# Performance work log

Hardware: AMD Instinct MI355X
Metric: run time of the kernel (lower is better)

The kernel has to match this reference:

```python
import jax, jax.numpy as jnp
import numpy as np

N, E, C, NB = 10000, 160000, 32, 8  # atoms, edges, channels, radial basis


def _W(k, shp):
    return jax.random.normal(k, shp, jnp.float32) / np.float32(np.sqrt(shp[0]))


def setup_inputs():
    ks = jax.random.split(jax.random.key(0), 16)
    return {
        "p1": jax.random.normal(ks[0], (N, C), jnp.float32),
        "p3": jax.random.normal(ks[1], (N, 3, C), jnp.float32),
        "r3": jax.random.normal(ks[2], (E, 3), jnp.float32),
        "basis": jax.random.normal(ks[3], (E, NB), jnp.float32),
        "idx_i": jax.random.randint(ks[4], (E,), 0, N, jnp.int32),
        "idx_j": jax.random.randint(ks[5], (E,), 0, N, jnp.int32),
        "pp1_W": _W(ks[6], (C, C)), "pp1_b": jnp.zeros((C,), jnp.float32),
        "pi1_W1": _W(ks[7], (2 * C, C)), "pi1_b1": jnp.zeros((C,), jnp.float32),
        "pi1_W2": _W(ks[8], (C, 3 * C)), "pi1_b2": jnp.zeros((3 * C,), jnp.float32),
        "pi1_W3": _W(ks[9], (3 * C, 3 * C * NB)),
        "ii1_W": _W(ks[10], (C, C)), "ii1_b": jnp.zeros((C,), jnp.float32),
        "pp3_W": _W(ks[11], (C, C)), "pp3_b": jnp.zeros((C,), jnp.float32),
        "pi3_W1": _W(ks[12], (2 * C, C)), "pi3_b1": jnp.zeros((C,), jnp.float32),
        "pi3_W2": _W(ks[13], (C, C)), "pi3_b2": jnp.zeros((C,), jnp.float32),
        "pi3_W3": _W(ks[14], (C, C * NB)),
        "ii3_W": _W(ks[15], (C, C)), "ii3_b": jnp.zeros((C,), jnp.float32),
    }


def _pi_layer(prop, idx_i, idx_j, basis, W1, b1, W2, b2, W3, out_c):
    # gather both endpoints, concat, linear MLP (no activation, no last bias),
    # contract trailing basis axis with per-edge basis functions
    inter = jnp.concatenate([prop[idx_i], prop[idx_j]], axis=-1)  # [E, ..., 2C]
    h = inter @ W1 + b1
    h = h @ W2 + b2
    h = h @ W3                                   # [E, ..., out_c*NB]
    h = h.reshape(h.shape[:-1] + (out_c, NB))
    return jnp.einsum('e...cb,eb->e...c', h, basis)


def _forward(p1, p3, r3, basis, idx_i, idx_j,
             pp1_W, pp1_b, pi1_W1, pi1_b1, pi1_W2, pi1_b2, pi1_W3, ii1_W, ii1_b,
             pp3_W, pp3_b, pi3_W1, pi3_b1, pi3_W2, pi3_b2, pi3_W3, ii3_W, ii3_b):
    act = jnp.tanh
    # rank-1 branch
    p1h = act(p1 @ pp1_W + pp1_b)                                   # [N, C]
    i1 = _pi_layer(p1h, idx_i, idx_j, basis,
                   pi1_W1, pi1_b1, pi1_W2, pi1_b2, pi1_W3, 3 * C)   # [E, 3C]
    i1_1, i1_2, i1_3 = jnp.split(i1, 3, axis=-1)
    i1a = act(i1_1 @ ii1_W + ii1_b)                                  # [E, C]
    p1n = jax.ops.segment_sum(i1a, idx_j, num_segments=N)            # [N, C]
    # rank-3 (vector) branch
    p3h = act(p3 @ pp3_W + pp3_b)                                    # [N, 3, C]
    i3 = _pi_layer(p3h, idx_i, idx_j, basis,
                   pi3_W1, pi3_b1, pi3_W2, pi3_b2, pi3_W3, C)        # [E, 3, C]
    i3 = act(i3 @ ii3_W + ii3_b)
    # equivariant scale/add: i3*i1_2 + r3*i1_3 (broadcast over Cartesian axis)
    i3 = i3 * i1_2[:, None, :] + r3[:, :, None] * i1_3[:, None, :]   # [E, 3, C]
    p3n = jax.ops.segment_sum(i3, idx_j, num_segments=N)             # [N, 3, C]
    # dot layer + residual into p1, then rescale p3 by p1
    p1o = jnp.sum(p3n * p3n, axis=1) + p1n                           # [N, C]
    p3o = p3n * p1o[:, None, :]                                      # [N, 3, C]
    return p1o, p3o


def reference(p1, p3, r3, basis, idx_i, idx_j,
              pp1_W, pp1_b, pi1_W1, pi1_b1, pi1_W2, pi1_b2, pi1_W3, ii1_W, ii1_b,
              pp3_W, pp3_b, pi3_W1, pi3_b1, pi3_W2, pi3_b2, pi3_W3, ii3_W, ii3_b):
    return _forward(p1, p3, r3, basis, idx_i, idx_j,
                    pp1_W, pp1_b, pi1_W1, pi1_b1, pi1_W2, pi1_b2, pi1_W3, ii1_W, ii1_b,
                    pp3_W, pp3_b, pi3_W1, pi3_b1, pi3_W2, pi3_b2, pi3_W3, ii3_W, ii3_b)
```

## Files before the change

### kernel.cpp

```cpp
#include <hip/hip_runtime.h>
#include <math.h>

#define NN 10000
#define NE 160000

typedef __attribute__((ext_vector_type(8))) short s8v;
typedef __attribute__((ext_vector_type(4))) float f4v;
typedef unsigned short u16;

#define OFF_P1HB 0u
#define OFF_P3HB 640000u
#define OFF_WB   2560000u
#define OFF_SCR  2703360u
#define OFF_P1N  2736640u
#define OFF_P3N  4016640u

#define OWF1  0
#define OBB1  49152
#define OII1T 52224
#define OWF3  53248
#define OBB3  69632
#define OII3T 70656
#define NWB   71680

__device__ __forceinline__ short f2b(float f) {
    unsigned u = __float_as_uint(f);
    u += 0x7fffu + ((u >> 16) & 1u);
    return (short)(u >> 16);
}
__device__ __forceinline__ float tanhf_fast(float x) {
    float xc = fminf(9.f, fmaxf(-9.f, x));
    float e = __expf(2.f * xc);
    return (e - 1.f) * __builtin_amdgcn_rcpf(e + 1.f);
}

__global__ __launch_bounds__(256) void node_prep(
    const float* __restrict__ p1, const float* __restrict__ p3,
    const float* __restrict__ pp1_W, const float* __restrict__ pp1_b,
    const float* __restrict__ pp3_W, const float* __restrict__ pp3_b,
    u16* __restrict__ p1hb, u16* __restrict__ p3hb)
{
    __shared__ float Ws[2][32 * 32];
    __shared__ float bsm[2][32];
    int tid = threadIdx.x;
    for (int i = tid; i < 32 * 32; i += 256) { Ws[0][i] = pp1_W[i]; Ws[1][i] = pp3_W[i]; }
    if (tid < 32) { bsm[0][tid] = pp1_b[tid]; bsm[1][tid] = pp3_b[tid]; }
    __syncthreads();
    int idx = blockIdx.x * 256 + tid;
    int n = idx >> 7;
    int r = (idx >> 5) & 3;
    int c = idx & 31;
    int sel = (r == 0) ? 0 : 1;
    const float* in = (r == 0) ? (p1 + n * 32) : (p3 + (n * 3 + (r - 1)) * 32);
    float acc = bsm[sel][c];
    #pragma unroll
    for (int k = 0; k < 32; ++k) acc += in[k] * Ws[sel][k * 32 + c];
    short v = f2b(tanhf(acc));
    if (r == 0) p1hb[n * 32 + c] = (u16)v;
    else        p3hb[(n * 3 + (r - 1)) * 32 + c] = (u16)v;
}

__global__ __launch_bounds__(256) void wprep1(
    const float* __restrict__ W1, const float* __restrict__ W2,
    const float* __restrict__ b1, const float* __restrict__ b2,
    const float* __restrict__ W13, const float* __restrict__ W23,
    const float* __restrict__ b13, const float* __restrict__ b23,
    float* __restrict__ scr)
{
    float* T1  = scr;
    float* T3  = scr + 6144;
    float* bt1 = scr + 8192;
    float* bt3 = scr + 8288;
    int i = blockIdx.x * 256 + threadIdx.x;
    if (i < 6144) {
        int r = i / 96, c = i % 96;
        float a = 0.f;
        #pragma unroll 8
        for (int k = 0; k < 32; ++k) a += W1[r * 32 + k] * W2[k * 96 + c];
        T1[i] = a;
    } else if ((i -= 6144) < 2048) {
        int r = i / 32, c = i % 32;
        float a = 0.f;
        #pragma unroll 8
        for (int k = 0; k < 32; ++k) a += W13[r * 32 + k] * W23[k * 32 + c];
        T3[i] = a;
    } else if ((i -= 2048) < 96) {
        float a = b2[i];
        #pragma unroll 8
        for (int k = 0; k < 32; ++k) a += b1[k] * W2[k * 96 + i];
        bt1[i] = a;
    } else if ((i -= 96) < 32) {
        float a = b23[i];
        #pragma unroll 8
        for (int k = 0; k < 32; ++k) a += b13[k] * W23[k * 32 + i];
        bt3[i] = a;
    }
}

__global__ __launch_bounds__(256) void wprep2(
    const float* __restrict__ W3, const float* __restrict__ W33,
    const float* __restrict__ ii1, const float* __restrict__ ii3,
    const float* __restrict__ scr, u16* __restrict__ wb)
{
    const float* T1  = scr;
    const float* T3  = scr + 6144;
    const float* bt1 = scr + 8192;
    const float* bt3 = scr + 8288;
    int i0 = blockIdx.x * 256 + threadIdx.x;
    if (i0 >= NWB) return;
    int i = i0;
    float v = 0.f;
    if (i < 49152) {
        int b = i / 6144, r = i % 6144;
        int nt = r / 1024, r2 = r % 1024;
        int ks = r2 / 512, r3 = r2 & 511;
        int L = r3 >> 3, j = r3 & 7;
        int k = ks * 32 + (L >> 4) * 8 + j;
        int c = 16 * nt + (L & 15);
        float a = 0.f;
        #pragma unroll 8
        for (int q = 0; q < 96; ++q) a += T1[k * 96 + q] * W3[q * 768 + c * 8 + b];
        v = a;
    } else if ((i -= 49152) < 3072) {
        int nt = i / 512, r3 = i & 511;
        int L = r3 >> 3, j = r3 & 7;
        if ((L >> 4) == 0) {
            int x = (16 * nt + (L & 15)) * 8 + j;
            float a = 0.f;
            #pragma unroll 8
            for (int q = 0; q < 96; ++q) a += bt1[q] * W3[q * 768 + x];
            v = a;
        }
    } else if ((i -= 3072) < 1024) {
        int nt = i / 512, r3 = i & 511;
        int L = r3 >> 3, j = r3 & 7;
        v = ii1[((L >> 4) * 8 + j) * 32 + 16 * nt + (L & 15)];
    } else if ((i -= 1024) < 16384) {
        int b = i / 2048, r = i % 2048;
        int nt = r / 1024, r2 = r % 1024;
        int ks = r2 / 512, r3 = r2 & 511;
        int L = r3 >> 3, j = r3 & 7;
        int k = ks * 32 + (L >> 4) * 8 + j;
        int c = 16 * nt + (L & 15);
        float a = 0.f;
        #pragma unroll 8
        for (int q = 0; q < 32; ++q) a += T3[k * 32 + q] * W33[q * 256 + c * 8 + b];
        v = a;
    } else if ((i -= 16384) < 1024) {
        int nt = i / 512, r3 = i & 511;
        int L = r3 >> 3, j = r3 & 7;
        if ((L >> 4) == 0) {
            int x = (16 * nt + (L & 15)) * 8 + j;
            float a = 0.f;
            #pragma unroll 8
            for (int q = 0; q < 32; ++q) a += bt3[q] * W33[q * 256 + x];
            v = a;
        }
    } else {
        i -= 1024;
        int nt = i / 512, r3 = i & 511;
        int L = r3 >> 3, j = r3 & 7;
        v = ii3[((L >> 4) * 8 + j) * 32 + 16 * nt + (L & 15)];
    }
    wb[i0] = (u16)f2b(v);
}

__global__ __launch_bounds__(64, 3) void edge_kernel(
    const u16* __restrict__ p1hb, const u16* __restrict__ p3hb,
    const float* __restrict__ r3, const float* __restrict__ basis,
    const int* __restrict__ idx_i, const int* __restrict__ idx_j,
    const u16* __restrict__ wb,
    const float* __restrict__ ii1b, const float* __restrict__ ii3b,
    float* __restrict__ p1n, float* __restrict__ p3n)
{
    __shared__ int4 smem4[192];
    char* sw = (char*)smem4;
    int*   sIdxI = (int*)(sw + 0);
    int*   sIdxJ = (int*)(sw + 128);
    float* sBasT = (float*)(sw + 256);
    float* sR3   = (float*)(sw + 1280);
    u16*   sT2   = (u16*)(sw + 1664);

    const int l   = threadIdx.x & 63;
    const int r16 = l & 15;
    const int kg  = l >> 4;
    const int ebase = blockIdx.x * 32;

    if (l < 32) sIdxI[l] = idx_i[ebase + l];
    else        sIdxJ[l - 32] = idx_j[ebase + l - 32];
    {
        int e = l & 31, hf = l >> 5;
        const float4* bp = (const float4*)(basis + (size_t)(ebase + e) * 8);
        float4 q = bp[hf];
        sBasT[(4 * hf + 0) * 32 + e] = q.x;
        sBasT[(4 * hf + 1) * 32 + e] = q.y;
        sBasT[(4 * hf + 2) * 32 + e] = q.z;
        sBasT[(4 * hf + 3) * 32 + e] = q.w;
        if (hf == 0) {
            sR3[e]      = r3[(size_t)(ebase + e) * 3 + 0];
            sR3[32 + e] = r3[(size_t)(ebase + e) * 3 + 1];
            sR3[64 + e] = r3[(size_t)(ebase + e) * 3 + 2];
        }
    }

    const float vii1[2] = { ii1b[r16], ii1b[16 + r16] };
    const float vii3[2] = { ii3b[r16], ii3b[16 + r16] };

    const f4v zf = {0.f, 0.f, 0.f, 0.f};

    s8v bA[2];
    #pragma unroll
    for (int m = 0; m < 2; ++m) {
        s8v t;
        #pragma unroll
        for (int j = 0; j < 8; ++j)
            t[j] = (kg == 0) ? f2b(sBasT[j * 32 + m * 16 + r16]) : (short)0;
        bA[m] = t;
    }

    s8v avI[2], avJ[2];
    #pragma unroll
    for (int m = 0; m < 2; ++m) {
        int rowA = m * 16 + r16;
        avI[m] = *(const s8v*)(p1hb + (size_t)sIdxI[rowA] * 32 + kg * 8);
        avJ[m] = *(const s8v*)(p1hb + (size_t)sIdxJ[rowA] * 32 + kg * 8);
    }

    f4v accT[2][6];
    {
        const u16* gBB = wb + OBB1;
        #pragma unroll
        for (int nt = 0; nt < 6; ++nt) {
            s8v bbv = *(const s8v*)(gBB + (nt * 64 + l) * 8);
            #pragma unroll
            for (int m = 0; m < 2; ++m)
                accT[m][nt] = __builtin_amdgcn_mfma_f32_16x16x32_bf16(bA[m], bbv, zf, 0, 0, 0);
        }
    }

    {
        const u16* gW = wb + OWF1;
        #pragma unroll 2
        for (int b = 0; b < 8; ++b) {
            float tb[2][4];
            #pragma unroll
            for (int m = 0; m < 2; ++m)
                #pragma unroll
                for (int rr = 0; rr < 4; ++rr)
                    tb[m][rr] = sBasT[b * 32 + m * 16 + 4 * kg + rr];
            #pragma unroll
            for (int nt = 0; nt < 6; ++nt) {
                const u16* bp = gW + ((size_t)(b * 6 + nt) * 2) * 512 + l * 8;
                s8v bv0 = *(const s8v*)(bp);
                s8v bv1 = *(const s8v*)(bp + 512);
                #pragma unroll
                for (int m = 0; m < 2; ++m) {
                    f4v D = __builtin_amdgcn_mfma_f32_16x16x32_bf16(avI[m], bv0, zf, 0, 0, 0);
                    D = __builtin_amdgcn_mfma_f32_16x16x32_bf16(avJ[m], bv1, D, 0, 0, 0);
                    #pragma unroll
                    for (int rr = 0; rr < 4; ++rr)
                        accT[m][nt][rr] += tb[m][rr] * D[rr];
                }
            }
        }
    }

    {
        const u16* gII = wb + OII1T;
        #pragma unroll
        for (int m = 0; m < 2; ++m) {
            #pragma unroll
            for (int nt = 0; nt < 2; ++nt)
                #pragma unroll
                for (int rr = 0; rr < 4; ++rr)
                    sT2[(4 * kg + rr) * 40 + 16 * nt + r16] = (u16)f2b(accT[m][nt][rr]);
            s8v av = *(const s8v*)(sT2 + r16 * 40 + 8 * kg);
            #pragma unroll
            for (int nt = 0; nt < 2; ++nt) {
                s8v bv = *(const s8v*)(gII + (nt * 64 + l) * 8);
                f4v ia = __builtin_amdgcn_mfma_f32_16x16x32_bf16(av, bv, zf, 0, 0, 0);
                #pragma unroll
                for (int rr = 0; rr < 4; ++rr) {
                    int rowD = m * 16 + 4 * kg + rr;
                    atomicAdd(&p1n[(size_t)sIdxJ[rowD] * 32 + 16 * nt + r16],
                              tanhf_fast(ia[rr] + vii1[nt]));
                }
            }
        }
    }

    const u16* gW3  = wb + OWF3;
    const u16* gBB3 = wb + OBB3;
    const u16* gII3 = wb + OII3T;
    for (int d = 0; d < 3; ++d) {
        s8v avI3[2], avJ3[2];
        #pragma unroll
        for (int m = 0; m < 2; ++m) {
            int rowA = m * 16 + r16;
            avI3[m] = *(const s8v*)(p3hb + ((size_t)sIdxI[rowA] * 3 + d) * 32 + kg * 8);
            avJ3[m] = *(const s8v*)(p3hb + ((size_t)sIdxJ[rowA] * 3 + d) * 32 + kg * 8);
        }
        f4v accP[2][2];
        #pragma unroll
        for (int nt = 0; nt < 2; ++nt) {
            s8v bbv = *(const s8v*)(gBB3 + (nt * 64 + l) * 8);
            #pragma unroll
            for (int m = 0; m < 2; ++m)
                accP[m][nt] = __builtin_amdgcn_mfma_f32_16x16x32_bf16(bA[m], bbv, zf, 0, 0, 0);
        }
        #pragma unroll 2
        for (int b = 0; b < 8; ++b) {
            float tb[2][4];
            #pragma unroll
            for (int m = 0; m < 2; ++m)
                #pragma unroll
                for (int rr = 0; rr < 4; ++rr)
                    tb[m][rr] = sBasT[b * 32 + m * 16 + 4 * kg + rr];
            #pragma unroll
            for (int nt = 0; nt < 2; ++nt) {
                const u16* bp = gW3 + ((size_t)(b * 2 + nt) * 2) * 512 + l * 8;
                s8v bv0 = *(const s8v*)(bp);
                s8v bv1 = *(const s8v*)(bp + 512);
                #pragma unroll
                for (int m = 0; m < 2; ++m) {
                    f4v D = __builtin_amdgcn_mfma_f32_16x16x32_bf16(avI3[m], bv0, zf, 0, 0, 0);
                    D = __builtin_amdgcn_mfma_f32_16x16x32_bf16(avJ3[m], bv1, D, 0, 0, 0);
                    #pragma unroll
                    for (int rr = 0; rr < 4; ++rr)
                        accP[m][nt][rr] += tb[m][rr] * D[rr];
                }
            }
        }
        #pragma unroll
        for (int m = 0; m < 2; ++m) {
            #pragma unroll
            for (int nt = 0; nt < 2; ++nt)
                #pragma unroll
                for (int rr = 0; rr < 4; ++rr)
                    sT2[(4 * kg + rr) * 40 + 16 * nt + r16] = (u16)f2b(accP[m][nt][rr]);
            s8v av = *(const s8v*)(sT2 + r16 * 40 + 8 * kg);
            #pragma unroll
            for (int nt = 0; nt < 2; ++nt) {
                s8v bv = *(const s8v*)(gII3 + (nt * 64 + l) * 8);
                f4v ja = __builtin_amdgcn_mfma_f32_16x16x32_bf16(av, bv, zf, 0, 0, 0);
                #pragma unroll
                for (int rr = 0; rr < 4; ++rr) {
                    int rowD = m * 16 + 4 * kg + rr;
                    float i3a = tanhf_fast(ja[rr] + vii3[nt]);
                    float val = i3a * accT[m][2 + nt][rr] + sR3[d * 32 + rowD] * accT[m][4 + nt][rr];
                    atomicAdd(&p3n[((size_t)sIdxJ[rowD] * 3 + d) * 32 + 16 * nt + r16], val);
                }
            }
        }
    }
}

__global__ __launch_bounds__(256) void finalize_kernel(
    const float* __restrict__ p1n, const float* __restrict__ p3n,
    float* __restrict__ out)
{
    int t = blockIdx.x * 256 + threadIdx.x;
    int n = t >> 5, c = t & 31;
    float a0 = p3n[(n * 3 + 0) * 32 + c];
    float a1 = p3n[(n * 3 + 1) * 32 + c];
    float a2 = p3n[(n * 3 + 2) * 32 + c];
    float p1o = p1n[t] + a0 * a0 + a1 * a1 + a2 * a2;
    out[t] = p1o;
    float* o3 = out + NN * 32;
    o3[(n * 3 + 0) * 32 + c] = a0 * p1o;
    o3[(n * 3 + 1) * 32 + c] = a1 * p1o;
    o3[(n * 3 + 2) * 32 + c] = a2 * p1o;
}

extern "C" void kernel_launch(void* const* d_in, const int* in_sizes, int n_in,
                              void* d_out, int out_size, void* d_ws, size_t ws_size,
                              hipStream_t stream) {
    const float* p1     = (const float*)d_in[0];
    const float* p3     = (const float*)d_in[1];
    const float* r3     = (const float*)d_in[2];
    const float* basis  = (const float*)d_in[3];
    const int*   idx_i  = (const int*)d_in[4];
    const int*   idx_j  = (const int*)d_in[5];
    const float* pp1_W  = (const float*)d_in[6];
    const float* pp1_b  = (const float*)d_in[7];
    const float* pi1_W1 = (const float*)d_in[8];
    const float* pi1_b1 = (const float*)d_in[9];
    const float* pi1_W2 = (const float*)d_in[10];
    const float* pi1_b2 = (const float*)d_in[11];
    const float* pi1_W3 = (const float*)d_in[12];
    const float* ii1_W  = (const float*)d_in[13];
    const float* ii1_b  = (const float*)d_in[14];
    const float* pp3_W  = (const float*)d_in[15];
    const float* pp3_b  = (const float*)d_in[16];
    const float* pi3_W1 = (const float*)d_in[17];
    const float* pi3_b1 = (const float*)d_in[18];
    const float* pi3_W2 = (const float*)d_in[19];
    const float* pi3_b2 = (const float*)d_in[20];
    const float* pi3_W3 = (const float*)d_in[21];
    const float* ii3_W  = (const float*)d_in[22];
    const float* ii3_b  = (const float*)d_in[23];

    char* ws = (char*)d_ws;
    u16*   p1hb = (u16*)(ws + OFF_P1HB);
    u16*   p3hb = (u16*)(ws + OFF_P3HB);
    u16*   wb   = (u16*)(ws + OFF_WB);
    float* scr  = (float*)(ws + OFF_SCR);
    float* p1n  = (float*)(ws + OFF_P1N);
    float* p3n  = (float*)(ws + OFF_P3N);

    hipMemsetAsync(p1n, 0, 5120000, stream);

    node_prep<<<dim3(5000), dim3(256), 0, stream>>>(p1, p3, pp1_W, pp1_b, pp3_W, pp3_b, p1hb, p3hb);
    wprep1<<<dim3(33), dim3(256), 0, stream>>>(
        pi1_W1, pi1_W2, pi1_b1, pi1_b2, pi3_W1, pi3_W2, pi3_b1, pi3_b2, scr);
    wprep2<<<dim3(NWB / 256), dim3(256), 0, stream>>>(
        pi1_W3, pi3_W3, ii1_W, ii3_W, scr, wb);

    edge_kernel<<<dim3(NE / 32), dim3(64), 0, stream>>>(
        p1hb, p3hb, r3, basis, idx_i, idx_j, wb,
        ii1_b, ii3_b, p1n, p3n);

    finalize_kernel<<<dim3(1250), dim3(256), 0, stream>>>(p1n, p3n, (float*)d_out);
}
```

Before: 136.9 us.

## Fuse node prep, weight folding and accumulator zeroing into one prep kernel

Merges the node projection kernel, the two weight-folding kernels and the memset into a single launch, with block ranges handling each job. The weight folding is reassociated as W1·(W2·W3 column slice) per block using shared memory, which removes the scratch round-trip and the dependency between wprep1 and wprep2. The aim is to cut launch and serialization overhead ahead of the edge kernel. The cost is a larger shared allocation per block, which can lower occupancy for the node-prep blocks, and more complex indexing.

Measured after the change: 133.1 us. 2.8% less time.

```diff
diff --git a/kernel.cpp b/kernel.cpp
--- a/kernel.cpp
+++ b/kernel.cpp
@@ -11,7 +11,6 @@
 #define OFF_P1HB 0u
 #define OFF_P3HB 640000u
 #define OFF_WB   2560000u
-#define OFF_SCR  2703360u
 #define OFF_P1N  2736640u
 #define OFF_P3N  4016640u
 
@@ -34,135 +33,163 @@
     return (e - 1.f) * __builtin_amdgcn_rcpf(e + 1.f);
 }
 
-__global__ __launch_bounds__(256) void node_prep(
+__global__ __launch_bounds__(256) void prep_kernel(
     const float* __restrict__ p1, const float* __restrict__ p3,
     const float* __restrict__ pp1_W, const float* __restrict__ pp1_b,
     const float* __restrict__ pp3_W, const float* __restrict__ pp3_b,
-    u16* __restrict__ p1hb, u16* __restrict__ p3hb)
+    const float* __restrict__ W1, const float* __restrict__ W2,
+    const float* __restrict__ W3,
+    const float* __restrict__ b1v, const float* __restrict__ b2v,
+    const float* __restrict__ ii1,
+    const float* __restrict__ W13, const float* __restrict__ W23,
+    const float* __restrict__ W33,
+    const float* __restrict__ b13v, const float* __restrict__ b23v,
+    const float* __restrict__ ii3,
+    u16* __restrict__ p1hb, u16* __restrict__ p3hb,
+    u16* __restrict__ wb, float* __restrict__ p1n)
 {
-    __shared__ float Ws[2][32 * 32];
-    __shared__ float bsm[2][32];
-    int tid = threadIdx.x;
-    for (int i = tid; i < 32 * 32; i += 256) { Ws[0][i] = pp1_W[i]; Ws[1][i] = pp3_W[i]; }
-    if (tid < 32) { bsm[0][tid] = pp1_b[tid]; bsm[1][tid] = pp3_b[tid]; }
-    __syncthreads();
-    int idx = blockIdx.x * 256 + tid;
-    int n = idx >> 7;
-    int r = (idx >> 5) & 3;
-    int c = idx & 31;
-    int sel = (r == 0) ? 0 : 1;
-    const float* in = (r == 0) ? (p1 + n * 32) : (p3 + (n * 3 + (r - 1)) * 32);
-    float acc = bsm[sel][c];
-    #pragma unroll
-    for (int k = 0; k < 32; ++k) acc += in[k] * Ws[sel][k * 32 + c];
-    short v = f2b(tanhf(acc));
-    if (r == 0) p1hb[n * 32 + c] = (u16)v;
-    else        p3hb[(n * 3 + (r - 1)) * 32 + c] = (u16)v;
-}
-
-__global__ __launch_bounds__(256) void wprep1(
-    const float* __restrict__ W1, const float* __restrict__ W2,
-    const float* __restrict__ b1, const float* __restrict__ b2,
-    const float* __restrict__ W13, const float* __restrict__ W23,
-    const float* __restrict__ b13, const float* __restrict__ b23,
-    float* __restrict__ scr)
-{
-    float* T1  = scr;
-    float* T3  = scr + 6144;
-    float* bt1 = scr + 8192;
-    float* bt3 = scr + 8288;
-    int i = blockIdx.x * 256 + threadIdx.x;
-    if (i < 6144) {
-        int r = i / 96, c = i % 96;
-        float a = 0.f;
-        #pragma unroll 8
-        for (int k = 0; k < 32; ++k) a += W1[r * 32 + k] * W2[k * 96 + c];
-        T1[i] = a;
-    } else if ((i -= 6144) < 2048) {
-        int r = i / 32, c = i % 32;
-        float a = 0.f;
-        #pragma unroll 8
-        for (int k = 0; k < 32; ++k) a += W13[r * 32 + k] * W23[k * 32 + c];
-        T3[i] = a;
-    } else if ((i -= 2048) < 96) {
-        float a = b2[i];
-        #pragma unroll 8
-        for (int k = 0; k < 32; ++k) a += b1[k] * W2[k * 96 + i];
-        bt1[i] = a;
-    } else if ((i -= 96) < 32) {
-        float a = b23[i];
-        #pragma unroll 8
-        for (int k = 0; k < 32; ++k) a += b13[k] * W23[k * 32 + i];
-        bt3[i] = a;
-    }
-}
-
-__global__ __launch_bounds__(256) void wprep2(
-    const float* __restrict__ W3, const float* __restrict__ W33,
-    const float* __restrict__ ii1, const float* __restrict__ ii3,
-    const float* __restrict__ scr, u16* __restrict__ wb)
-{
-    const float* T1  = scr;
-    const float* T3  = scr + 6144;
-    const float* bt1 = scr + 8192;
-    const float* bt3 = scr + 8288;
-    int i0 = blockIdx.x * 256 + threadIdx.x;
-    if (i0 >= NWB) return;
-    int i = i0;
-    float v = 0.f;
-    if (i < 49152) {
-        int b = i / 6144, r = i % 6144;
-        int nt = r / 1024, r2 = r % 1024;
-        int ks = r2 / 512, r3 = r2 & 511;
-        int L = r3 >> 3, j = r3 & 7;
-        int k = ks * 32 + (L >> 4) * 8 + j;
-        int c = 16 * nt + (L & 15);
-        float a = 0.f;
-        #pragma unroll 8
-        for (int q = 0; q < 96; ++q) a += T1[k * 96 + q] * W3[q * 768 + c * 8 + b];
-        v = a;
-    } else if ((i -= 49152) < 3072) {
-        int nt = i / 512, r3 = i & 511;
-        int L = r3 >> 3, j = r3 & 7;
-        if ((L >> 4) == 0) {
-            int x = (16 * nt + (L & 15)) * 8 + j;
+    __shared__ float smem[6912];
+    const int blk = blockIdx.x;
+    const int tid = threadIdx.x;
+
+    if (blk < 5000) {
+        float* Ws0 = smem;
+        float* Ws1 = smem + 1024;
+        float* bs0 = smem + 2048;
+        float* bs1 = smem + 2080;
+        for (int i = tid; i < 1024; i += 256) { Ws0[i] = pp1_W[i]; Ws1[i] = pp3_W[i]; }
+        if (tid < 32) { bs0[tid] = pp1_b[tid]; bs1[tid] = pp3_b[tid]; }
+        __syncthreads();
+        int idx = blk * 256 + tid;
+        int n = idx >> 7;
+        int r = (idx >> 5) & 3;
+        int c = idx & 31;
+        const float* Ws = (r == 0) ? Ws0 : Ws1;
+        const float* bs = (r == 0) ? bs0 : bs1;
+        const float* in = (r == 0) ? (p1 + n * 32) : (p3 + (n * 3 + (r - 1)) * 32);
+        float acc = bs[c];
+        #pragma unroll
+        for (int k = 0; k < 32; ++k) acc += in[k] * Ws[k * 32 + c];
+        short v = f2b(tanhf(acc));
+        if (r == 0) p1hb[n * 32 + c] = (u16)v;
+        else        p3hb[(n * 3 + (r - 1)) * 32 + c] = (u16)v;
+    } else if (blk < 5064) {
+        const int cb0 = (blk - 5000) * 12;
+        float* sW1  = smem;
+        float* sW2  = smem + 2048;
+        float* sW3c = smem + 5120;
+        float* sU   = smem + 6272;
+        float* sbt  = smem + 6656;
+        for (int i = tid; i < 2048; i += 256) sW1[i] = W1[i];
+        for (int i = tid; i < 3072; i += 256) sW2[i] = W2[i];
+        for (int i = tid; i < 1152; i += 256) {
+            int q = i / 12, u = i % 12;
+            sW3c[i] = W3[q * 768 + cb0 + u];
+        }
+        __syncthreads();
+        for (int t = tid; t < 480; t += 256) {
+            if (t < 384) {
+                int c2 = t / 12, u = t % 12;
+                float a = 0.f;
+                #pragma unroll 8
+                for (int q = 0; q < 96; ++q) a += sW2[c2 * 96 + q] * sW3c[q * 12 + u];
+                sU[t] = a;
+            } else {
+                int q = t - 384;
+                float a = b2v[q];
+                #pragma unroll 8
+                for (int c2 = 0; c2 < 32; ++c2) a += b1v[c2] * sW2[c2 * 96 + q];
+                sbt[q] = a;
+            }
+        }
+        __syncthreads();
+        for (int o = tid; o < 768; o += 256) {
+            int k = o / 12, u = o % 12;
             float a = 0.f;
             #pragma unroll 8
-            for (int q = 0; q < 96; ++q) a += bt1[q] * W3[q * 768 + x];
-            v = a;
-        }
-    } else if ((i -= 3072) < 1024) {
-        int nt = i / 512, r3 = i & 511;
-        int L = r3 >> 3, j = r3 & 7;
-        v = ii1[((L >> 4) * 8 + j) * 32 + 16 * nt + (L & 15)];
-    } else if ((i -= 1024) < 16384) {
-        int b = i / 2048, r = i % 2048;
-        int nt = r / 1024, r2 = r % 1024;
-        int ks = r2 / 512, r3 = r2 & 511;
-        int L = r3 >> 3, j = r3 & 7;
-        int k = ks * 32 + (L >> 4) * 8 + j;
-        int c = 16 * nt + (L & 15);
-        float a = 0.f;
-        #pragma unroll 8
-        for (int q = 0; q < 32; ++q) a += T3[k * 32 + q] * W33[q * 256 + c * 8 + b];
-        v = a;
-    } else if ((i -= 16384) < 1024) {
-        int nt = i / 512, r3 = i & 511;
-        int L = r3 >> 3, j = r3 & 7;
-        if ((L >> 4) == 0) {
-            int x = (16 * nt + (L & 15)) * 8 + j;
+            for (int c2 = 0; c2 < 32; ++c2) a += sW1[k * 32 + c2] * sU[c2 * 12 + u];
+            int cb = cb0 + u, b = cb & 7, c = cb >> 3;
+            int nt = c >> 4, cL = c & 15;
+            int ks = k >> 5, k5 = k & 31, Lhi = k5 >> 3, j = k5 & 7;
+            wb[OWF1 + b * 6144 + nt * 1024 + ks * 512 + (Lhi * 16 + cL) * 8 + j] = (u16)f2b(a);
+        }
+        for (int o = tid; o < 48; o += 256) {
+            int u = o >> 2, Lhi = o & 3;
+            int x = cb0 + u;
+            float a = 0.f;
+            if (Lhi == 0) {
+                #pragma unroll 8
+                for (int q = 0; q < 96; ++q) a += sbt[q] * sW3c[q * 12 + u];
+            }
+            int j = x & 7, c = x >> 3, nt = c >> 4, cL = c & 15;
+            wb[OBB1 + nt * 512 + (Lhi * 16 + cL) * 8 + j] = (u16)f2b(a);
+        }
+    } else if (blk < 5096) {
+        const int cb0 = (blk - 5064) * 8;
+        float* sW13  = smem;
+        float* sW23  = smem + 2048;
+        float* sW33c = smem + 3072;
+        float* sU3   = smem + 3328;
+        float* sbt3  = smem + 3584;
+        for (int i = tid; i < 2048; i += 256) sW13[i] = W13[i];
+        for (int i = tid; i < 1024; i += 256) sW23[i] = W23[i];
+        for (int i = tid; i < 256; i += 256) {
+            int q = i / 8, u = i % 8;
+            sW33c[i] = W33[q * 256 + cb0 + u];
+        }
+        __syncthreads();
+        for (int t = tid; t < 288; t += 256) {
+            if (t < 256) {
+                int c2 = t / 8, u = t % 8;
+                float a = 0.f;
+                #pragma unroll 8
+                for (int q = 0; q < 32; ++q) a += sW23[c2 * 32 + q] * sW33c[q * 8 + u];
+                sU3[t] = a;
+            } else {
+                int q = t - 256;
+                float a = b23v[q];
+                #pragma unroll 8
+                for (int c2 = 0; c2 < 32; ++c2) a += b13v[c2] * sW23[c2 * 32 + q];
+                sbt3[q] = a;
+            }
+        }
+        __syncthreads();
+        for (int o = tid; o < 512; o += 256) {
+            int k = o / 8, u = o % 8;
             float a = 0.f;
             #pragma unroll 8
-            for (int q = 0; q < 32; ++q) a += bt3[q] * W33[q * 256 + x];
-            v = a;
+            for (int c2 = 0; c2 < 32; ++c2) a += sW13[k * 32 + c2] * sU3[c2 * 8 + u];
+            int cb = cb0 + u, b = cb & 7, c = cb >> 3;
+            int nt = c >> 4, cL = c & 15;
+            int ks = k >> 5, k5 = k & 31, Lhi = k5 >> 3, j = k5 & 7;
+            wb[OWF3 + b * 2048 + nt * 1024 + ks * 512 + (Lhi * 16 + cL) * 8 + j] = (u16)f2b(a);
+        }
+        for (int o = tid; o < 32; o += 256) {
+            int u = o >> 2, Lhi = o & 3;
+            int x = cb0 + u;
+            float a = 0.f;
+            if (Lhi == 0) {
+                #pragma unroll
+                for (int q = 0; q < 32; ++q) a += sbt3[q] * sW33c[q * 8 + u];
+            }
+            int j = x & 7, c = x >> 3, nt = c >> 4, cL = c & 15;
+            wb[OBB3 + nt * 512 + (Lhi * 16 + cL) * 8 + j] = (u16)f2b(a);
+        }
+    } else if (blk == 5096) {
+        for (int i = tid; i < 2048; i += 256) {
+            if (i < 1024) {
+                int nt = i >> 9, L = (i >> 3) & 63, j = i & 7;
+                wb[OII1T + i] = (u16)f2b(ii1[((L >> 4) * 8 + j) * 32 + 16 * nt + (L & 15)]);
+            } else {
+                int i2 = i - 1024;
+                int nt = i2 >> 9, L = (i2 >> 3) & 63, j = i2 & 7;
+                wb[OII3T + i2] = (u16)f2b(ii3[((L >> 4) * 8 + j) * 32 + 16 * nt + (L & 15)]);
+            }
         }
     } else {
-        i -= 1024;
-        int nt = i / 512, r3 = i & 511;
-        int L = r3 >> 3, j = r3 & 7;
-        v = ii3[((L >> 4) * 8 + j) * 32 + 16 * nt + (L & 15)];
-    }
-    wb[i0] = (u16)f2b(v);
+        float4 z = make_float4(0.f, 0.f, 0.f, 0.f);
+        ((float4*)p1n)[(size_t)(blk - 5097) * 256 + tid] = z;
+    }
 }
 
 __global__ __launch_bounds__(64, 3) void edge_kernel(
@@ -404,17 +431,14 @@
     u16*   p1hb = (u16*)(ws + OFF_P1HB);
     u16*   p3hb = (u16*)(ws + OFF_P3HB);
     u16*   wb   = (u16*)(ws + OFF_WB);
-    float* scr  = (float*)(ws + OFF_SCR);
     float* p1n  = (float*)(ws + OFF_P1N);
     float* p3n  = (float*)(ws + OFF_P3N);
 
-    hipMemsetAsync(p1n, 0, 5120000, stream);
-
-    node_prep<<<dim3(5000), dim3(256), 0, stream>>>(p1, p3, pp1_W, pp1_b, pp3_W, pp3_b, p1hb, p3hb);
-    wprep1<<<dim3(33), dim3(256), 0, stream>>>(
-        pi1_W1, pi1_W2, pi1_b1, pi1_b2, pi3_W1, pi3_W2, pi3_b1, pi3_b2, scr);
-    wprep2<<<dim3(NWB / 256), dim3(256), 0, stream>>>(
-        pi1_W3, pi3_W3, ii1_W, ii3_W, scr, wb);
+    prep_kernel<<<dim3(6347), dim3(256), 0, stream>>>(
+        p1, p3, pp1_W, pp1_b, pp3_W, pp3_b,
+        pi1_W1, pi1_W2, pi1_W3, pi1_b1, pi1_b2, ii1_W,
+        pi3_W1, pi3_W2, pi3_W3, pi3_b1, pi3_b2, ii3_W,
+        p1hb, p3hb, wb, p1n);
 
     edge_kernel<<<dim3(NE / 32), dim3(64), 0, stream>>>(
         p1hb, p3hb, r3, basis, idx_i, idx_j, wb,
```
